# Kernel optimization log

Measured on AMD Instinct MI355X. Metric: run time of the kernel, lower is better.

## Reference

```python
import jax, jax.numpy as jnp
import numpy as np

B, T, S, E, D = 16, 1024, 1024, 1024, 1024  # batch, trg_len, src_len, enc_dim, trg_dim

def setup_inputs() -> dict:
    key = jax.random.key(0)
    k1, k2, k3, k4, k5 = jax.random.split(key, 5)
    sc = 0.02
    return {
        "hidden": jax.random.normal(k1, (B, T, D), dtype=jnp.float32),
        "encoder_outputs": jax.random.normal(k2, (B, S, E), dtype=jnp.float32),
        "W_attn": jax.random.normal(k3, (D, E), dtype=jnp.float32) * sc,
        "b_attn": jax.random.normal(k4, (D,), dtype=jnp.float32) * sc,
        "W_out": jax.random.normal(k5, (D, E + D), dtype=jnp.float32) * sc,
    }

def reference(hidden, encoder_outputs, W_attn, b_attn, W_out):
    # score, method='general': energies = Linear(enc_out) ; bmm(hidden, energies^T)
    proj = jnp.einsum('bse,de->bsd', encoder_outputs, W_attn) + b_attn  # (B,S,D)
    attn_energies = jnp.einsum('btd,bsd->bts', hidden, proj)            # (B,T,S)
    attn_weights = jax.nn.softmax(attn_energies, axis=-1)               # (B,T,S)
    weighted_context = jnp.einsum('bts,bse->bte', attn_weights, encoder_outputs)  # (B,T,E)
    h_cat = jnp.concatenate([weighted_context, hidden], axis=-1)        # (B,T,E+D)
    h_tilde = jnp.tanh(jnp.einsum('btc,dc->btd', h_cat, W_out))         # (B,T,D)
    return h_tilde, attn_weights, attn_energies
```

## Files before the change

kernel.cpp:

```cpp
#include <hip/hip_runtime.h>
#include <stdint.h>


typedef __bf16 bf16x8 __attribute__((ext_vector_type(8)));
typedef float  f32x4  __attribute__((ext_vector_type(4)));

enum { MODE_PROJ = 0, MODE_ENERGY = 1, MODE_WC = 2, MODE_OUT = 3 };

__device__ __forceinline__ ushort f2bf(float f) {
    uint32_t u = __builtin_bit_cast(uint32_t, f);
    u += 0x7fffu + ((u >> 16) & 1u);
    return (ushort)(u >> 16);
}

#define GLB_PTR(p) ((const __attribute__((address_space(1))) void*)(p))
#define LDS_PTR(p) ((__attribute__((address_space(3))) void*)(p))

__device__ __forceinline__ void stage_tile(const ushort* __restrict__ g, int ld,
                                           ushort* lds, int wave, int lane) {
#pragma unroll
    for (int i = 0; i < 4; ++i) {
        const int seg  = i * 4 + wave;
        const int p    = seg * 1024 + lane * 16;
        const int row  = p >> 7;
        const int cpos = (p >> 4) & 7;
        const int csrc = cpos ^ (row & 7);
        const ushort* gp = g + (size_t)row * ld + csrc * 8;
        __builtin_amdgcn_global_load_lds(GLB_PTR(gp), LDS_PTR((char*)lds + seg * 1024), 16, 0, 0);
    }
}

template <int MODE>
__global__ __launch_bounds__(256) void gemm_bt(
    const ushort* __restrict__ A0, const ushort* __restrict__ A1,
    const ushort* __restrict__ B0, const float* __restrict__ bias,
    ushort* __restrict__ out_bf, float* __restrict__ out_f)
{
    constexpr int    KTOT   = (MODE == MODE_OUT) ? 2048 : 1024;
    constexpr int    LDB    = (MODE == MODE_OUT) ? 2048 : 1024;
    constexpr int    NT     = KTOT / 64;
    constexpr size_t BBATCH = (MODE == MODE_ENERGY || MODE == MODE_WC) ? ((size_t)1 << 20) : 0;

    const int flat = (blockIdx.z * 8 + blockIdx.y) * 8 + blockIdx.x;
    const int nid  = ((flat & 7) << 7) | (flat >> 3);
    const int b    = nid >> 6;
    const int bm   = ((nid >> 3) & 7) << 7;
    const int bn   = (nid & 7) << 7;

    const int wave = threadIdx.x >> 6;
    const int lane = threadIdx.x & 63;
    const int wm   = wave >> 1;
    const int wn   = wave & 1;

    const ushort* Ab0 = A0 + ((size_t)b << 20) + (size_t)bm * 1024;
    const ushort* Ab1 = nullptr;
    if constexpr (MODE == MODE_OUT) Ab1 = A1 + ((size_t)b << 20) + (size_t)bm * 1024;
    const ushort* Bb0 = B0 + (size_t)b * BBATCH + (size_t)bn * LDB;

    __shared__ ushort ldsA[2][128 * 64];
    __shared__ ushort ldsB[2][128 * 64];

    f32x4 acc[4][4];
#pragma unroll
    for (int r = 0; r < 4; ++r)
#pragma unroll
        for (int c = 0; c < 4; ++c) acc[r][c] = f32x4{0.f, 0.f, 0.f, 0.f};

    auto stage_step = [&](int t, int buf) {
        const int k0 = t * 64;
        const ushort* Ag; int kA;
        if constexpr (MODE == MODE_OUT) { Ag = (k0 < 1024) ? Ab0 : Ab1; kA = k0 & 1023; }
        else                            { Ag = Ab0;                     kA = k0; }
        stage_tile(Ag + kA, 1024, ldsA[buf], wave, lane);
        stage_tile(Bb0 + k0, LDB,  ldsB[buf], wave, lane);
    };

    auto compute_step = [&](int buf) {
#pragma unroll
        for (int ks = 0; ks < 2; ++ks) {
            const int quad = lane >> 4;
            const int l15  = lane & 15;
            bf16x8 af[4], bfr[4];
#pragma unroll
            for (int r = 0; r < 4; ++r) {
                const int row   = wm * 64 + r * 16 + l15;
                const int chunk = ks * 4 + quad;
                af[r] = *(const bf16x8*)&ldsA[buf][row * 64 + ((chunk ^ (row & 7)) * 8)];
            }
#pragma unroll
            for (int c = 0; c < 4; ++c) {
                const int row   = wn * 64 + c * 16 + l15;
                const int chunk = ks * 4 + quad;
                bfr[c] = *(const bf16x8*)&ldsB[buf][row * 64 + ((chunk ^ (row & 7)) * 8)];
            }
#pragma unroll
            for (int r = 0; r < 4; ++r)
#pragma unroll
                for (int c = 0; c < 4; ++c)
                    acc[r][c] = __builtin_amdgcn_mfma_f32_16x16x32_bf16(af[r], bfr[c], acc[r][c], 0, 0, 0);
        }
    };

    stage_step(0, 0);
    __syncthreads();

    for (int t = 0; t < NT; t += 2) {
        stage_step(t + 1, 1);
        compute_step(0);
        __syncthreads();
        if (t + 2 < NT) stage_step(t + 2, 0);
        compute_step(1);
        __syncthreads();
    }

    const size_t obase = (size_t)b << 20;
    const int quad = lane >> 4;
    const int l15  = lane & 15;
#pragma unroll
    for (int r = 0; r < 4; ++r) {
#pragma unroll
        for (int c = 0; c < 4; ++c) {
#pragma unroll
            for (int g = 0; g < 4; ++g) {
                const int row = bm + wm * 64 + r * 16 + quad * 4 + g;
                const int col = bn + wn * 64 + c * 16 + l15;
                float v = acc[r][c][g];
                const size_t idx = obase + (size_t)row * 1024 + col;
                if constexpr (MODE == MODE_PROJ) {
                    out_bf[idx] = f2bf(v + bias[col]);
                } else if constexpr (MODE == MODE_ENERGY) {
                    out_f[idx] = v;
                } else if constexpr (MODE == MODE_WC) {
                    out_bf[idx] = f2bf(v);
                } else {
                    out_f[idx] = tanhf(v);
                }
            }
        }
    }
}

__global__ __launch_bounds__(256) void conv_k(const float* __restrict__ in,
                                              ushort* __restrict__ out) {
    const size_t i = (size_t)blockIdx.x * 256 + threadIdx.x;
    float4 v = ((const float4*)in)[i];
    ushort4 o;
    o.x = f2bf(v.x); o.y = f2bf(v.y); o.z = f2bf(v.z); o.w = f2bf(v.w);
    ((ushort4*)out)[i] = o;
}

__global__ __launch_bounds__(256) void transconv_k(const float* __restrict__ in,
                                                   ushort* __restrict__ outT,
                                                   ushort* __restrict__ outN) {
    __shared__ ushort t[64][65];
    const int b  = blockIdx.z;
    const int s0 = blockIdx.y * 64, e0 = blockIdx.x * 64;
    const float* ip = in   + ((size_t)b << 20);
    ushort*      tp = outT + ((size_t)b << 20);
    ushort*      np = outN + ((size_t)b << 20);
    const int tx = threadIdx.x & 15;
    const int ty = threadIdx.x >> 4;
#pragma unroll
    for (int i = 0; i < 4; ++i) {
        const int s = ty + i * 16;
        float4 v = *(const float4*)&ip[(size_t)(s0 + s) * 1024 + e0 + tx * 4];
        ushort4 n4;
        n4.x = f2bf(v.x); n4.y = f2bf(v.y); n4.z = f2bf(v.z); n4.w = f2bf(v.w);
        *(ushort4*)&np[(size_t)(s0 + s) * 1024 + e0 + tx * 4] = n4;
        t[tx * 4 + 0][s] = n4.x; t[tx * 4 + 1][s] = n4.y;
        t[tx * 4 + 2][s] = n4.z; t[tx * 4 + 3][s] = n4.w;
    }
    __syncthreads();
#pragma unroll
    for (int i = 0; i < 4; ++i) {
        const int e = ty + i * 16;
        ushort4 v;
        v.x = t[e][tx * 4 + 0]; v.y = t[e][tx * 4 + 1];
        v.z = t[e][tx * 4 + 2]; v.w = t[e][tx * 4 + 3];
        *(ushort4*)&tp[(size_t)(e0 + e) * 1024 + s0 + tx * 4] = v;
    }
}

__global__ __launch_bounds__(256) void softmax_k(const float* __restrict__ en,
                                                 float* __restrict__ w,
                                                 ushort* __restrict__ wbf) {
    const size_t row = blockIdx.x;
    const float* e = en + (row << 10);
    const int tid = threadIdx.x;
    const int wv = tid >> 6, ln = tid & 63;

    float4 v = ((const float4*)e)[tid];
    float m = fmaxf(fmaxf(v.x, v.y), fmaxf(v.z, v.w));
#pragma unroll
    for (int o = 32; o; o >>= 1) m = fmaxf(m, __shfl_xor(m, o, 64));
    __shared__ float sm[4];
    if (!ln) sm[wv] = m;
    __syncthreads();
    m = fmaxf(fmaxf(sm[0], sm[1]), fmaxf(sm[2], sm[3]));

    const float e0 = expf(v.x - m), e1 = expf(v.y - m), e2 = expf(v.z - m), e3 = expf(v.w - m);
    float s = e0 + e1 + e2 + e3;
#pragma unroll
    for (int o = 32; o; o >>= 1) s += __shfl_xor(s, o, 64);
    __shared__ float ss[4];
    if (!ln) ss[wv] = s;
    __syncthreads();
    s = ss[0] + ss[1] + ss[2] + ss[3];
    const float inv = 1.0f / s;

    const float w0 = e0 * inv, w1 = e1 * inv, w2 = e2 * inv, w3 = e3 * inv;
    ((float4*)(w + (row << 10)))[tid] = float4{w0, w1, w2, w3};
    ushort4 o4;
    o4.x = f2bf(w0); o4.y = f2bf(w1); o4.z = f2bf(w2); o4.w = f2bf(w3);
    ((ushort4*)(wbf + (row << 10)))[tid] = o4;
}

extern "C" void kernel_launch(void* const* d_in, const int* in_sizes, int n_in,
                              void* d_out, int out_size, void* d_ws, size_t ws_size,
                              hipStream_t stream) {
    (void)in_sizes; (void)n_in; (void)out_size; (void)ws_size;
    const float* hidden = (const float*)d_in[0];
    const float* enc    = (const float*)d_in[1];
    const float* Wattn  = (const float*)d_in[2];
    const float* battn  = (const float*)d_in[3];
    const float* Wout   = (const float*)d_in[4];

    const size_t M16 = (size_t)16 * 1024 * 1024;
    float* out_h = (float*)d_out;
    float* out_w = out_h + M16;
    float* out_e = out_w + M16;

    ushort* ws = (ushort*)d_ws;
    ushort* hidden_bf = ws;
    ushort* encwc_bf  = ws + M16;
    ushort* proj_bf   = ws + 2 * M16;
    ushort* wattn_bf  = ws + 3 * M16;
    ushort* wout_bf   = ws + 3 * M16 + (1u << 20);
    ushort* encT_bf   = (ushort*)out_h;
    ushort* weights_bf = (ushort*)out_h + M16;

    dim3 blk(256, 1, 1);
    dim3 gG(8, 8, 16);
    dim3 gT(16, 16, 16);

    conv_k<<<dim3(16384), blk, 0, stream>>>(hidden, hidden_bf);
    conv_k<<<dim3(1024),  blk, 0, stream>>>(Wattn, wattn_bf);
    conv_k<<<dim3(2048),  blk, 0, stream>>>(Wout, wout_bf);
    transconv_k<<<gT, blk, 0, stream>>>(enc, encT_bf, encwc_bf);
    gemm_bt<MODE_PROJ><<<gG, blk, 0, stream>>>(encwc_bf, nullptr, wattn_bf, battn,
                                               proj_bf, nullptr);
    gemm_bt<MODE_ENERGY><<<gG, blk, 0, stream>>>(hidden_bf, nullptr, proj_bf, nullptr,
                                                 nullptr, out_e);
    softmax_k<<<dim3(16 * 1024), blk, 0, stream>>>(out_e, out_w, weights_bf);
    gemm_bt<MODE_WC><<<gG, blk, 0, stream>>>(weights_bf, nullptr, encT_bf, nullptr,
                                             encwc_bf, nullptr);
    gemm_bt<MODE_OUT><<<gG, blk, 0, stream>>>(encwc_bf, hidden_bf, wout_bf, nullptr,
                                              nullptr, out_h);
}
```

Baseline: 581.3 us.

## Deepen GEMM LDS pipeline to four stages with explicit vmcnt waits

Replaces the two-buffer LDS double-buffering with a four-buffer ring that keeps three tiles of global-to-LDS loads in flight. Each step waits on a partial vmcnt before a raw s_barrier, instead of a full __syncthreads drain. It also raises wave priority around the MFMA block with s_setprio. The aim is to hide global load latency better, at the cost of doubling LDS use (128 KB per block), which may lower occupancy.

Measured after the change: 702.6 us. 20.9% more time.

```diff
diff --git a/kernel.cpp b/kernel.cpp
--- a/kernel.cpp
+++ b/kernel.cpp
@@ -15,6 +15,7 @@
 
 #define GLB_PTR(p) ((const __attribute__((address_space(1))) void*)(p))
 #define LDS_PTR(p) ((__attribute__((address_space(3))) void*)(p))
+#define VMW(N) asm volatile("s_waitcnt vmcnt(" #N ")" ::: "memory")
 
 __device__ __forceinline__ void stage_tile(const ushort* __restrict__ g, int ld,
                                            ushort* lds, int wave, int lane) {
@@ -57,8 +58,8 @@
     if constexpr (MODE == MODE_OUT) Ab1 = A1 + ((size_t)b << 20) + (size_t)bm * 1024;
     const ushort* Bb0 = B0 + (size_t)b * BBATCH + (size_t)bn * LDB;
 
-    __shared__ ushort ldsA[2][128 * 64];
-    __shared__ ushort ldsB[2][128 * 64];
+    __shared__ ushort ldsA[4][128 * 64];
+    __shared__ ushort ldsB[4][128 * 64];
 
     f32x4 acc[4][4];
 #pragma unroll
@@ -93,24 +94,39 @@
                 const int chunk = ks * 4 + quad;
                 bfr[c] = *(const bf16x8*)&ldsB[buf][row * 64 + ((chunk ^ (row & 7)) * 8)];
             }
+            __builtin_amdgcn_s_setprio(1);
 #pragma unroll
             for (int r = 0; r < 4; ++r)
 #pragma unroll
                 for (int c = 0; c < 4; ++c)
                     acc[r][c] = __builtin_amdgcn_mfma_f32_16x16x32_bf16(af[r], bfr[c], acc[r][c], 0, 0, 0);
+            __builtin_amdgcn_s_setprio(0);
         }
     };
 
     stage_step(0, 0);
-    __syncthreads();
-
-    for (int t = 0; t < NT; t += 2) {
-        stage_step(t + 1, 1);
-        compute_step(0);
-        __syncthreads();
-        if (t + 2 < NT) stage_step(t + 2, 0);
-        compute_step(1);
-        __syncthreads();
+    stage_step(1, 1);
+    stage_step(2, 2);
+    VMW(16);
+    __builtin_amdgcn_sched_barrier(0);
+    __builtin_amdgcn_s_barrier();
+    __builtin_amdgcn_sched_barrier(0);
+
+    for (int t = 0; t < NT; t += 4) {
+#pragma unroll
+        for (int j = 0; j < 4; ++j) {
+            const int s = t + j;
+            if (s + 3 < NT) stage_step(s + 3, (j + 3) & 3);
+            compute_step(j);
+            if (s < NT - 1) {
+                if (s + 4 <= NT)      { VMW(16); }
+                else if (s + 3 <= NT) { VMW(8);  }
+                else                  { VMW(0);  }
+                __builtin_amdgcn_sched_barrier(0);
+                __builtin_amdgcn_s_barrier();
+                __builtin_amdgcn_sched_barrier(0);
+            }
+        }
     }
 
     const size_t obase = (size_t)b << 20;
```
